# Kernel optimization log

Measured on AMD Instinct MI355X. Metric: run time of the kernel, lower is better.

The kernel has to match this reference:

```python
import jax, jax.numpy as jnp
import numpy as np

N_NODES = 50000
NEG_SLOPE = 0.01  # F.leaky_relu default


def setup_inputs() -> dict:
    key = jax.random.key(0)
    k1, k2, k3, k4, k5 = jax.random.split(key, 5)
    in_dim, out_dim, n_edges = 256, 64, 800000
    h = jax.random.normal(k1, (N_NODES, in_dim), dtype=jnp.float32)
    edge_src = jax.random.randint(k2, (n_edges,), 0, N_NODES, dtype=jnp.int32)
    edge_dst = jax.random.randint(k3, (n_edges,), 0, N_NODES, dtype=jnp.int32)
    W_fc = jax.random.normal(k4, (in_dim, out_dim), dtype=jnp.float32) / np.sqrt(in_dim)
    a_attn = jax.random.normal(k5, (2 * out_dim,), dtype=jnp.float32) / np.sqrt(2 * out_dim)
    return {"h": h, "edge_src": edge_src, "edge_dst": edge_dst, "W_fc": W_fc, "a_attn": a_attn}


def reference(h, edge_src, edge_dst, W_fc, a_attn):
    # z = fc(h)
    z = h @ W_fc                                   # [N, D]
    D = z.shape[1]
    # cat([z_src, z_dst]) @ a == z_src @ a_l + z_dst @ a_r (no edge concat materialized)
    a_l, a_r = a_attn[:D], a_attn[D:]
    s_l = z @ a_l                                  # [N]
    s_r = z @ a_r                                  # [N]
    e = s_l[edge_src] + s_r[edge_dst]              # [E]
    e = jnp.where(e > 0, e, NEG_SLOPE * e)         # leaky_relu
    # segment softmax over incoming edges of each dst node (DGL mailbox softmax)
    m = jax.ops.segment_max(e, edge_dst, num_segments=N_NODES)   # -inf for isolated nodes
    ex = jnp.exp(e - m[edge_dst])                  # [E]
    den = jax.ops.segment_sum(ex, edge_dst, num_segments=N_NODES)
    alpha = ex / den[edge_dst]                     # [E]
    # weighted neighbor aggregation: h_v = sum_{u->v} alpha * z_u
    msgs = alpha[:, None] * z[edge_src]            # [E, D]
    h_out = jax.ops.segment_sum(msgs, edge_dst, num_segments=N_NODES)  # [N, D]
    return h_out
```

## Files before the change

### kernel.cpp

```cpp
#include <hip/hip_runtime.h>

#define IN_DIM   256
#define OUT_DIM  64
#define NEG_SLOPE 0.01f
#define KPAD (IN_DIM + 8)
#define MAXBUCK 2048
#define CAP     1024
#define EPB     4096

typedef __attribute__((ext_vector_type(8))) short short8;
typedef __attribute__((ext_vector_type(4))) float f32x4;
typedef unsigned short ushort_t;

__device__ inline short f2bf(float f) {
    unsigned u = __float_as_uint(f);
    return (short)((u + 0x7FFF + ((u >> 16) & 1)) >> 16);
}
__device__ inline float bf2f(unsigned u16) { return __uint_as_float(u16 << 16); }

__global__ __launch_bounds__(256)
void prep_kernel(const float* __restrict__ W, short* __restrict__ Wt,
                 int* __restrict__ cnt, int nbuck)
{
    for (int i = threadIdx.x; i < nbuck; i += 256) cnt[i] = 0;
    for (int i = threadIdx.x; i < IN_DIM * OUT_DIM; i += 256) {
        const int k = i & (IN_DIM - 1);
        const int n = i >> 8;
        Wt[i] = f2bf(W[(size_t)k * OUT_DIM + n]);
    }
}

__global__ __launch_bounds__(256, 4)
void fused_kernel(const float* __restrict__ h, const short* __restrict__ Wt,
                  const float* __restrict__ a_attn,
                  ushort_t* __restrict__ z_bf, float* __restrict__ s_l,
                  float* __restrict__ s_r,
                  const int* __restrict__ esrc, const int* __restrict__ edst,
                  int* __restrict__ cnt, unsigned* __restrict__ perm,
                  int n_nodes, int n_edges, int nbuck, int ms_blocks)
{
    __shared__ union {
        short As[64 * KPAD];
        struct { int hist[MAXBUCK]; int cur[MAXBUCK]; } m;
    } sm;

    const int tid = threadIdx.x;

    if ((int)blockIdx.x < ms_blocks) {
        for (int i = tid; i < nbuck; i += 256) sm.m.hist[i] = 0;
        __syncthreads();
        const int base = blockIdx.x * EPB;
        unsigned pw[EPB / 256];
#pragma unroll
        for (int j = 0; j < EPB / 256; ++j) {
            const int i = base + j * 256 + tid;
            unsigned w = 0xFFFFFFFFu;
            if (i < n_edges) {
                const int d = edst[i];
                w = ((unsigned)d << 16) | (unsigned)esrc[i];
                atomicAdd(&sm.m.hist[d >> 5], 1);
            }
            pw[j] = w;
        }
        __syncthreads();
        for (int i = tid; i < nbuck; i += 256) {
            const int hv = sm.m.hist[i];
            if (hv) sm.m.cur[i] = i * CAP + atomicAdd(&cnt[i], hv);
        }
        __syncthreads();
#pragma unroll
        for (int j = 0; j < EPB / 256; ++j) {
            const unsigned w = pw[j];
            if (w != 0xFFFFFFFFu) {
                const int bk = (int)(w >> 21);
                const int pos = atomicAdd(&sm.m.cur[bk], 1);
                if (pos < (bk + 1) * CAP) perm[pos] = w;
            }
        }
        return;
    }

    const int wave = tid >> 6;
    const int lane = tid & 63;
    const int nbase = ((int)blockIdx.x - ms_blocks) * 64;

    for (int i = tid; i < 64 * (IN_DIM / 4); i += 256) {
        const int m  = i >> 6;
        const int k4 = i & 63;
        int node = nbase + m;
        if (node >= n_nodes) node = n_nodes - 1;
        const float4 h4 = *(const float4*)&h[(size_t)node * IN_DIM + k4 * 4];
        short* dp = &sm.As[m * KPAD + k4 * 4];
        dp[0] = f2bf(h4.x); dp[1] = f2bf(h4.y);
        dp[2] = f2bf(h4.z); dp[3] = f2bf(h4.w);
    }
    __syncthreads();

    f32x4 acc[4];
#pragma unroll
    for (int t = 0; t < 4; ++t) acc[t] = (f32x4){0.f, 0.f, 0.f, 0.f};

    const int col0 = lane & 15;
    const int quad = lane >> 4;
    const int mrow = wave * 16 + col0;
    const int kq   = quad * 8;

#pragma unroll
    for (int ks = 0; ks < IN_DIM / 32; ++ks) {
        const int kb = ks * 32 + kq;
        const short8 a = *(const short8*)&sm.As[mrow * KPAD + kb];
#pragma unroll
        for (int t = 0; t < 4; ++t) {
            const short8 b = *(const short8*)&Wt[(t * 16 + col0) * IN_DIM + kb];
            acc[t] = __builtin_amdgcn_mfma_f32_16x16x32_bf16(a, b, acc[t], 0, 0, 0);
        }
    }

    float al[4], ar[4];
#pragma unroll
    for (int t = 0; t < 4; ++t) {
        al[t] = a_attn[t * 16 + col0];
        ar[t] = a_attn[OUT_DIM + t * 16 + col0];
    }
#pragma unroll
    for (int r = 0; r < 4; ++r) {
        const int m = nbase + wave * 16 + quad * 4 + r;
        const bool live = m < n_nodes;
        float sl = 0.f, sr = 0.f;
#pragma unroll
        for (int t = 0; t < 4; ++t) {
            const float v = acc[t][r];
            if (live) z_bf[(size_t)m * OUT_DIM + t * 16 + col0] = (ushort_t)f2bf(v);
            sl += v * al[t];
            sr += v * ar[t];
        }
#pragma unroll
        for (int off = 1; off < 16; off <<= 1) {
            sl += __shfl_xor(sl, off, 16);
            sr += __shfl_xor(sr, off, 16);
        }
        if (live && col0 == 0) { s_l[m] = sl; s_r[m] = sr; }
    }
}

__global__ __launch_bounds__(512)
void gather_kernel(const unsigned* __restrict__ perm, const int* __restrict__ cnt,
                   const float* __restrict__ s_l, const float* __restrict__ s_r,
                   const ushort_t* __restrict__ z_bf, float* __restrict__ out,
                   int n_nodes)
{
    __shared__ unsigned eds[CAP];
    __shared__ ushort_t srcs[CAP];
    __shared__ int hist[32], starts[33], cur[32];

    const int tid = threadIdx.x;
    const int b   = blockIdx.x;
    int nE = cnt[b];
    if (nE > CAP) nE = CAP;

    if (tid < 32) hist[tid] = 0;
    __syncthreads();

    for (int i = tid; i < nE; i += 512) {
        const unsigned p = perm[(size_t)b * CAP + i];
        eds[i] = p;
        atomicAdd(&hist[(p >> 16) & 31], 1);
    }
    __syncthreads();

    if (tid < 32) {
        const int v = hist[tid];
        int inc = v;
#pragma unroll
        for (int off = 1; off < 32; off <<= 1) {
            const int u = __shfl_up(inc, off, 32);
            if (tid >= off) inc += u;
        }
        starts[tid + 1] = inc;
        cur[tid] = inc - v;
        if (tid == 0) starts[0] = 0;
    }
    __syncthreads();

    for (int i = tid; i < nE; i += 512) {
        const unsigned p = eds[i];
        const int pos = atomicAdd(&cur[(p >> 16) & 31], 1);
        srcs[pos] = (ushort_t)(p & 0xFFFFu);
    }
    __syncthreads();

    const int ld = tid >> 4;
    const int c  = tid & 15;
    const int d  = b * 32 + ld;
    if (d >= n_nodes) return;

    int k = starts[ld];
    const int ke = starts[ld + 1];
    const float srd = s_r[d];

    float a0 = 0.f, a1 = 0.f, a2 = 0.f, a3 = 0.f, den = 0.f;
    for (; k + 4 <= ke; k += 4) {
        const int s0 = srcs[k],     s1 = srcs[k + 1];
        const int s2 = srcs[k + 2], s3 = srcs[k + 3];
        const float l0 = s_l[s0], l1 = s_l[s1], l2 = s_l[s2], l3 = s_l[s3];
        const uint2 q0 = *(const uint2*)&z_bf[(size_t)s0 * OUT_DIM + c * 4];
        const uint2 q1 = *(const uint2*)&z_bf[(size_t)s1 * OUT_DIM + c * 4];
        const uint2 q2 = *(const uint2*)&z_bf[(size_t)s2 * OUT_DIM + c * 4];
        const uint2 q3 = *(const uint2*)&z_bf[(size_t)s3 * OUT_DIM + c * 4];
        float e0 = l0 + srd, e1 = l1 + srd, e2 = l2 + srd, e3 = l3 + srd;
        e0 = e0 > 0.f ? e0 : NEG_SLOPE * e0;
        e1 = e1 > 0.f ? e1 : NEG_SLOPE * e1;
        e2 = e2 > 0.f ? e2 : NEG_SLOPE * e2;
        e3 = e3 > 0.f ? e3 : NEG_SLOPE * e3;
        const float x0 = __expf(e0), x1 = __expf(e1);
        const float x2 = __expf(e2), x3 = __expf(e3);
        den += (x0 + x1) + (x2 + x3);
        a0 += x0 * bf2f(q0.x & 0xFFFFu) + x1 * bf2f(q1.x & 0xFFFFu)
            + x2 * bf2f(q2.x & 0xFFFFu) + x3 * bf2f(q3.x & 0xFFFFu);
        a1 += x0 * bf2f(q0.x >> 16)     + x1 * bf2f(q1.x >> 16)
            + x2 * bf2f(q2.x >> 16)     + x3 * bf2f(q3.x >> 16);
        a2 += x0 * bf2f(q0.y & 0xFFFFu) + x1 * bf2f(q1.y & 0xFFFFu)
            + x2 * bf2f(q2.y & 0xFFFFu) + x3 * bf2f(q3.y & 0xFFFFu);
        a3 += x0 * bf2f(q0.y >> 16)     + x1 * bf2f(q1.y >> 16)
            + x2 * bf2f(q2.y >> 16)     + x3 * bf2f(q3.y >> 16);
    }
    for (; k < ke; ++k) {
        const int s0 = srcs[k];
        float e0 = s_l[s0] + srd;
        e0 = e0 > 0.f ? e0 : NEG_SLOPE * e0;
        const float x0 = __expf(e0);
        const uint2 q0 = *(const uint2*)&z_bf[(size_t)s0 * OUT_DIM + c * 4];
        den += x0;
        a0 += x0 * bf2f(q0.x & 0xFFFFu);
        a1 += x0 * bf2f(q0.x >> 16);
        a2 += x0 * bf2f(q0.y & 0xFFFFu);
        a3 += x0 * bf2f(q0.y >> 16);
    }
    const float inv = den > 0.f ? 1.f / den : 0.f;
    float4 o;
    o.x = a0 * inv; o.y = a1 * inv; o.z = a2 * inv; o.w = a3 * inv;
    *(float4*)&out[(size_t)d * OUT_DIM + c * 4] = o;
}

extern "C" void kernel_launch(void* const* d_in, const int* in_sizes, int n_in,
                              void* d_out, int out_size, void* d_ws, size_t ws_size,
                              hipStream_t stream)
{
    const float* h        = (const float*)d_in[0];
    const int*   edge_src = (const int*)  d_in[1];
    const int*   edge_dst = (const int*)  d_in[2];
    const float* W        = (const float*)d_in[3];
    const float* a_attn   = (const float*)d_in[4];
    float*       out      = (float*)d_out;

    const int n_nodes = in_sizes[0] / IN_DIM;
    const int n_edges = in_sizes[1];
    const int nbuck   = (n_nodes + 31) >> 5;

    char* wsb = (char*)d_ws;
    short*    Wt   = (short*)wsb;
    size_t off = (size_t)IN_DIM * OUT_DIM * sizeof(short);
    ushort_t* z_bf = (ushort_t*)(wsb + off);
    off += (size_t)n_nodes * OUT_DIM * sizeof(ushort_t);
    float*    s_l  = (float*)(wsb + off);  off += (size_t)n_nodes * 4;
    float*    s_r  = (float*)(wsb + off);  off += (size_t)n_nodes * 4;
    int*      cnt  = (int*)(wsb + off);    off += ((size_t)nbuck * 4 + 15) & ~(size_t)15;
    unsigned* perm = (unsigned*)(wsb + off);

    const int ms_blocks   = (n_edges + EPB - 1) / EPB;
    const int gemm_blocks = (n_nodes + 63) / 64;

    prep_kernel<<<1, 256, 0, stream>>>(W, Wt, cnt, nbuck);
    fused_kernel<<<ms_blocks + gemm_blocks, 256, 0, stream>>>(
        h, Wt, a_attn, z_bf, s_l, s_r, edge_src, edge_dst, cnt, perm,
        n_nodes, n_edges, nbuck, ms_blocks);
    gather_kernel<<<nbuck, 512, 0, stream>>>(
        perm, cnt, s_l, s_r, z_bf, out, n_nodes);
}
```

Baseline: 137.8 us.

## Replace per-destination sort in gather with edge-parallel LDS atomic accumulation

The gather kernel no longer counting-sorts edges by local destination. Instead, 16-lane groups walk the bucket's edges directly and accumulate weighted messages and denominators into a padded shared-memory array with float atomics, then normalize and write out. The aim is to drop two sorting passes and barriers and to remove load imbalance across destinations, at the cost of many LDS atomics and a changed summation order. Separately, the count reset moves to a memset, the weight transpose uses 8 blocks, and the bf16 conversion into LDS is packed into single 64-bit stores.

```diff
diff --git a/kernel.cpp b/kernel.cpp
--- a/kernel.cpp
+++ b/kernel.cpp
@@ -7,23 +7,24 @@
 #define MAXBUCK 2048
 #define CAP     1024
 #define EPB     4096
+#define ASTRIDE 65
 
 typedef __attribute__((ext_vector_type(8))) short short8;
 typedef __attribute__((ext_vector_type(4))) float f32x4;
 typedef unsigned short ushort_t;
 
-__device__ inline short f2bf(float f) {
+__device__ inline unsigned f2bf_u(float f) {
     unsigned u = __float_as_uint(f);
-    return (short)((u + 0x7FFF + ((u >> 16) & 1)) >> 16);
-}
+    return (u + 0x7FFF + ((u >> 16) & 1)) >> 16;
+}
+__device__ inline short f2bf(float f) { return (short)f2bf_u(f); }
 __device__ inline float bf2f(unsigned u16) { return __uint_as_float(u16 << 16); }
 
 __global__ __launch_bounds__(256)
-void prep_kernel(const float* __restrict__ W, short* __restrict__ Wt,
-                 int* __restrict__ cnt, int nbuck)
-{
-    for (int i = threadIdx.x; i < nbuck; i += 256) cnt[i] = 0;
-    for (int i = threadIdx.x; i < IN_DIM * OUT_DIM; i += 256) {
+void prep_kernel(const float* __restrict__ W, short* __restrict__ Wt)
+{
+    const int g = blockIdx.x * 256 + threadIdx.x;
+    for (int i = g; i < IN_DIM * OUT_DIM; i += 8 * 256) {
         const int k = i & (IN_DIM - 1);
         const int n = i >> 8;
         Wt[i] = f2bf(W[(size_t)k * OUT_DIM + n]);
@@ -90,9 +91,10 @@
         int node = nbase + m;
         if (node >= n_nodes) node = n_nodes - 1;
         const float4 h4 = *(const float4*)&h[(size_t)node * IN_DIM + k4 * 4];
-        short* dp = &sm.As[m * KPAD + k4 * 4];
-        dp[0] = f2bf(h4.x); dp[1] = f2bf(h4.y);
-        dp[2] = f2bf(h4.z); dp[3] = f2bf(h4.w);
+        uint2 p;
+        p.x = f2bf_u(h4.x) | (f2bf_u(h4.y) << 16);
+        p.y = f2bf_u(h4.z) | (f2bf_u(h4.w) << 16);
+        *(uint2*)&sm.As[m * KPAD + k4 * 4] = p;
     }
     __syncthreads();
 
@@ -143,103 +145,81 @@
     }
 }
 
-__global__ __launch_bounds__(512)
+__global__ __launch_bounds__(256)
 void gather_kernel(const unsigned* __restrict__ perm, const int* __restrict__ cnt,
                    const float* __restrict__ s_l, const float* __restrict__ s_r,
                    const ushort_t* __restrict__ z_bf, float* __restrict__ out,
                    int n_nodes)
 {
     __shared__ unsigned eds[CAP];
-    __shared__ ushort_t srcs[CAP];
-    __shared__ int hist[32], starts[33], cur[32];
+    __shared__ float accum[32 * ASTRIDE];
+    __shared__ float denS[32];
+    __shared__ float srS[32];
 
     const int tid = threadIdx.x;
     const int b   = blockIdx.x;
     int nE = cnt[b];
     if (nE > CAP) nE = CAP;
 
-    if (tid < 32) hist[tid] = 0;
+    for (int i = tid; i < 32 * ASTRIDE; i += 256) accum[i] = 0.f;
+    if (tid < 32) {
+        denS[tid] = 0.f;
+        const int d = b * 32 + tid;
+        srS[tid] = (d < n_nodes) ? s_r[d] : 0.f;
+    }
+    for (int i = tid; i < nE; i += 256) eds[i] = perm[(size_t)b * CAP + i];
     __syncthreads();
 
-    for (int i = tid; i < nE; i += 512) {
-        const unsigned p = perm[(size_t)b * CAP + i];
-        eds[i] = p;
-        atomicAdd(&hist[(p >> 16) & 31], 1);
-    }
-    __syncthreads();
-
-    if (tid < 32) {
-        const int v = hist[tid];
-        int inc = v;
-#pragma unroll
-        for (int off = 1; off < 32; off <<= 1) {
-            const int u = __shfl_up(inc, off, 32);
-            if (tid >= off) inc += u;
-        }
-        starts[tid + 1] = inc;
-        cur[tid] = inc - v;
-        if (tid == 0) starts[0] = 0;
-    }
-    __syncthreads();
-
-    for (int i = tid; i < nE; i += 512) {
-        const unsigned p = eds[i];
-        const int pos = atomicAdd(&cur[(p >> 16) & 31], 1);
-        srcs[pos] = (ushort_t)(p & 0xFFFFu);
-    }
-    __syncthreads();
-
-    const int ld = tid >> 4;
+    const int qw = tid >> 4;
     const int c  = tid & 15;
-    const int d  = b * 32 + ld;
-    if (d >= n_nodes) return;
-
-    int k = starts[ld];
-    const int ke = starts[ld + 1];
-    const float srd = s_r[d];
-
-    float a0 = 0.f, a1 = 0.f, a2 = 0.f, a3 = 0.f, den = 0.f;
-    for (; k + 4 <= ke; k += 4) {
-        const int s0 = srcs[k],     s1 = srcs[k + 1];
-        const int s2 = srcs[k + 2], s3 = srcs[k + 3];
-        const float l0 = s_l[s0], l1 = s_l[s1], l2 = s_l[s2], l3 = s_l[s3];
+
+    for (int i = qw; i < nE; i += 32) {
+        const int j = i + 16;
+        const bool v1 = j < nE;
+        const unsigned p0 = eds[i];
+        const unsigned p1 = v1 ? eds[j] : p0;
+        const int s0 = p0 & 0xFFFFu, ld0 = (p0 >> 16) & 31;
+        const int s1 = p1 & 0xFFFFu, ld1 = (p1 >> 16) & 31;
+        const float l0 = s_l[s0];
+        const float l1 = s_l[s1];
         const uint2 q0 = *(const uint2*)&z_bf[(size_t)s0 * OUT_DIM + c * 4];
         const uint2 q1 = *(const uint2*)&z_bf[(size_t)s1 * OUT_DIM + c * 4];
-        const uint2 q2 = *(const uint2*)&z_bf[(size_t)s2 * OUT_DIM + c * 4];
-        const uint2 q3 = *(const uint2*)&z_bf[(size_t)s3 * OUT_DIM + c * 4];
-        float e0 = l0 + srd, e1 = l1 + srd, e2 = l2 + srd, e3 = l3 + srd;
+        float e0 = l0 + srS[ld0];
+        float e1 = l1 + srS[ld1];
         e0 = e0 > 0.f ? e0 : NEG_SLOPE * e0;
         e1 = e1 > 0.f ? e1 : NEG_SLOPE * e1;
-        e2 = e2 > 0.f ? e2 : NEG_SLOPE * e2;
-        e3 = e3 > 0.f ? e3 : NEG_SLOPE * e3;
-        const float x0 = __expf(e0), x1 = __expf(e1);
-        const float x2 = __expf(e2), x3 = __expf(e3);
-        den += (x0 + x1) + (x2 + x3);
-        a0 += x0 * bf2f(q0.x & 0xFFFFu) + x1 * bf2f(q1.x & 0xFFFFu)
-            + x2 * bf2f(q2.x & 0xFFFFu) + x3 * bf2f(q3.x & 0xFFFFu);
-        a1 += x0 * bf2f(q0.x >> 16)     + x1 * bf2f(q1.x >> 16)
-            + x2 * bf2f(q2.x >> 16)     + x3 * bf2f(q3.x >> 16);
-        a2 += x0 * bf2f(q0.y & 0xFFFFu) + x1 * bf2f(q1.y & 0xFFFFu)
-            + x2 * bf2f(q2.y & 0xFFFFu) + x3 * bf2f(q3.y & 0xFFFFu);
-        a3 += x0 * bf2f(q0.y >> 16)     + x1 * bf2f(q1.y >> 16)
-            + x2 * bf2f(q2.y >> 16)     + x3 * bf2f(q3.y >> 16);
-    }
-    for (; k < ke; ++k) {
-        const int s0 = srcs[k];
-        float e0 = s_l[s0] + srd;
-        e0 = e0 > 0.f ? e0 : NEG_SLOPE * e0;
         const float x0 = __expf(e0);
-        const uint2 q0 = *(const uint2*)&z_bf[(size_t)s0 * OUT_DIM + c * 4];
-        den += x0;
-        a0 += x0 * bf2f(q0.x & 0xFFFFu);
-        a1 += x0 * bf2f(q0.x >> 16);
-        a2 += x0 * bf2f(q0.y & 0xFFFFu);
-        a3 += x0 * bf2f(q0.y >> 16);
-    }
-    const float inv = den > 0.f ? 1.f / den : 0.f;
-    float4 o;
-    o.x = a0 * inv; o.y = a1 * inv; o.z = a2 * inv; o.w = a3 * inv;
-    *(float4*)&out[(size_t)d * OUT_DIM + c * 4] = o;
+        const float x1 = __expf(e1);
+        float* r0 = &accum[ld0 * ASTRIDE + c * 4];
+        atomicAdd(&r0[0], x0 * bf2f(q0.x & 0xFFFFu));
+        atomicAdd(&r0[1], x0 * bf2f(q0.x >> 16));
+        atomicAdd(&r0[2], x0 * bf2f(q0.y & 0xFFFFu));
+        atomicAdd(&r0[3], x0 * bf2f(q0.y >> 16));
+        if (c == 0) atomicAdd(&denS[ld0], x0);
+        if (v1) {
+            float* r1 = &accum[ld1 * ASTRIDE + c * 4];
+            atomicAdd(&r1[0], x1 * bf2f(q1.x & 0xFFFFu));
+            atomicAdd(&r1[1], x1 * bf2f(q1.x >> 16));
+            atomicAdd(&r1[2], x1 * bf2f(q1.y & 0xFFFFu));
+            atomicAdd(&r1[3], x1 * bf2f(q1.y >> 16));
+            if (c == 0) atomicAdd(&denS[ld1], x1);
+        }
+    }
+    __syncthreads();
+
+    for (int i = tid; i < 32 * 16; i += 256) {
+        const int ld = i >> 4;
+        const int cq = i & 15;
+        const int d  = b * 32 + ld;
+        if (d < n_nodes) {
+            const float dn = denS[ld];
+            const float inv = dn > 0.f ? 1.f / dn : 0.f;
+            const float* r = &accum[ld * ASTRIDE + cq * 4];
+            float4 o;
+            o.x = r[0] * inv; o.y = r[1] * inv; o.z = r[2] * inv; o.w = r[3] * inv;
+            *(float4*)&out[(size_t)d * OUT_DIM + cq * 4] = o;
+        }
+    }
 }
 
 extern "C" void kernel_launch(void* const* d_in, const int* in_sizes, int n_in,
@@ -270,10 +250,11 @@
     const int ms_blocks   = (n_edges + EPB - 1) / EPB;
     const int gemm_blocks = (n_nodes + 63) / 64;
 
-    prep_kernel<<<1, 256, 0, stream>>>(W, Wt, cnt, nbuck);
+    hipMemsetAsync(cnt, 0, (size_t)nbuck * sizeof(int), stream);
+    prep_kernel<<<8, 256, 0, stream>>>(W, Wt);
     fused_kernel<<<ms_blocks + gemm_blocks, 256, 0, stream>>>(
         h, Wt, a_attn, z_bf, s_l, s_r, edge_src, edge_dst, cnt, perm,
         n_nodes, n_edges, nbuck, ms_blocks);
-    gather_kernel<<<nbuck, 512, 0, stream>>>(
+    gather_kernel<<<nbuck, 256, 0, stream>>>(
         perm, cnt, s_l, s_r, z_bf, out, n_nodes);
 }
```

Result: slower. 426.1 us (+209.3%).
